# Optimization experiments

Hardware: AMD Instinct MI355X
Metric: run time of the kernel (lower is better)

## Reference

```python
import jax, jax.numpy as jnp
import numpy as np

N = 50000        # nodes
E = 800000       # edges (avg degree 16)
IN = 256         # in_feature_dim
H = 4            # heads_num
F = 64           # out_feature_dim per head (H*F == IN)
NEG_SLOPE = 0.2  # LeakyReLU slope used for both scoring and output activation


def setup_inputs() -> dict:
    key = jax.random.key(0)
    ks = jax.random.split(key, 8)
    x = jax.random.normal(ks[0], (N, IN), dtype=jnp.float32)
    edge_src = jax.random.randint(ks[1], (E,), 0, N, dtype=jnp.int32)
    edge_trg = jax.random.randint(ks[2], (E,), 0, N, dtype=jnp.int32)
    # xavier-ish scaled params
    W = jax.random.normal(ks[3], (IN, H * F), dtype=jnp.float32) * 0.06
    a_src = jax.random.normal(ks[4], (H, F), dtype=jnp.float32) * 0.1
    a_trg = jax.random.normal(ks[5], (H, F), dtype=jnp.float32) * 0.1
    skip_w = jax.random.normal(ks[6], (IN, H * F), dtype=jnp.float32) * 0.06
    bias = jnp.zeros((H * F,), dtype=jnp.float32)
    return {"x": x, "W": W, "a_src": a_src, "a_trg": a_trg,
            "skip_w": skip_w, "bias": bias,
            "edge_src": edge_src, "edge_trg": edge_trg}


def _leaky(v):
    return jnp.where(v > 0, v, NEG_SLOPE * v)


def reference(x, W, a_src, a_trg, skip_w, bias, edge_src, edge_trg):
    n_nodes = x.shape[0]
    # node-wise projection: [N, H, F]
    proj = (x @ W).reshape(n_nodes, H, F)
    # per-head attention scores: [N, H]
    s_src = jnp.einsum('nhf,hf->nh', proj, a_src)
    s_trg = jnp.einsum('nhf,hf->nh', proj, a_trg)
    # lift to edges + LeakyReLU scoring: [E, H]
    e = _leaky(s_src[edge_src] + s_trg[edge_trg])
    # neighborhood-aware (scatter) softmax over incoming edges of each target
    e = e - jnp.max(e)                      # global max subtraction, as in the source
    ex = jnp.exp(e)
    denom = jax.ops.segment_sum(ex, edge_trg, num_segments=n_nodes)  # [N, H]
    attn = ex / (denom[edge_trg] + 1e-16)   # [E, H]
    # weighted aggregation: [E, H, F] -> scatter-add -> [N, H, F]
    weighted = proj[edge_src] * attn[..., None]
    out = jax.ops.segment_sum(weighted, edge_trg, num_segments=n_nodes)
    # skip connection (dims differ: in=256 vs per-head 64 -> use skip_proj)
    out = out + (x @ skip_w).reshape(n_nodes, H, F)
    # concat heads + bias + output activation (default LeakyReLU 0.2)
    out = out.reshape(n_nodes, H * F) + bias
    return _leaky(out)
```

## Files before the change

kernel.cpp:

```cpp
#include <hip/hip_runtime.h>
#include <math.h>

constexpr float SLOPE = 0.2f;

typedef __bf16 bf16x8 __attribute__((ext_vector_type(8)));
typedef __bf16 bf16x4 __attribute__((ext_vector_type(4)));
typedef float  f32x4  __attribute__((ext_vector_type(4)));

__device__ __forceinline__ int imin(int a, int b) { return a < b ? a : b; }

__device__ __forceinline__ void glds16(const void* g, void* l) {
    __builtin_amdgcn_global_load_lds(
        (const __attribute__((address_space(1))) unsigned int*)g,
        (__attribute__((address_space(3))) unsigned int*)l,
        16, 0, 0);
}

__global__ __launch_bounds__(256) void prep_k(
    const float* __restrict__ W, const float* __restrict__ skw,
    __bf16* __restrict__ Bt,
    const float* __restrict__ x, __bf16* __restrict__ xb, int nxv, int nxb,
    const int* __restrict__ etrg, int* __restrict__ cnt, int E)
{
    const int b = blockIdx.x;
    if (b < 512) {
        const int i = b * 256 + threadIdx.x;
        const int n = i >> 8, k = i & 255;
        const float v = (n < 256) ? W[k * 256 + n] : skw[k * 256 + (n - 256)];
        Bt[i] = (__bf16)v;
    } else if (b < 512 + nxb) {
        const int gid = (b - 512) * 256 + threadIdx.x;
        if (gid < nxv) {
            const float4 f0 = *(const float4*)(x + (size_t)gid * 8);
            const float4 f1 = *(const float4*)(x + (size_t)gid * 8 + 4);
            bf16x8 v;
            v[0] = (__bf16)f0.x; v[1] = (__bf16)f0.y;
            v[2] = (__bf16)f0.z; v[3] = (__bf16)f0.w;
            v[4] = (__bf16)f1.x; v[5] = (__bf16)f1.y;
            v[6] = (__bf16)f1.z; v[7] = (__bf16)f1.w;
            *(bf16x8*)(xb + (size_t)gid * 8) = v;
        }
    } else {
        const int e = (b - 512 - nxb) * 256 + threadIdx.x;
        if (e < E) atomicAdd(&cnt[etrg[e]], 1);
    }
}

__global__ __launch_bounds__(256, 2) void gemm_mfma(
    const __bf16* __restrict__ xb, const __bf16* __restrict__ Bt,
    __bf16* __restrict__ projb, float* __restrict__ out, int M)
{
    __shared__ __bf16 As[256 * 32];
    __shared__ __bf16 Bs[128 * 32];

    const int t    = threadIdx.x;
    const int w    = t >> 6;
    const int lane = t & 63;
    const int q    = lane >> 4;
    const int ln   = lane & 15;

    const int row0 = blockIdx.x * 256;
    const int bt0  = blockIdx.y * 128;

    f32x4 acc[4][8] = {};

    for (int k0 = 0; k0 < 256; k0 += 32) {
#pragma unroll
        for (int p = 0; p < 4; ++p) {
            const int idx = p * 256 + t;
            const int r   = idx >> 2;
            const int ko  = (idx & 3) * 8;
            const int ga  = imin(row0 + r, M - 1);
            glds16(xb + (size_t)ga * 256 + k0 + ko, &As[idx * 8]);
        }
#pragma unroll
        for (int p = 0; p < 2; ++p) {
            const int idx = p * 256 + t;
            const int r   = idx >> 2;
            const int ko  = (idx & 3) * 8;
            glds16(Bt + (size_t)(bt0 + r) * 256 + k0 + ko, &Bs[idx * 8]);
        }
        asm volatile("s_waitcnt vmcnt(0)" ::: "memory");
        __syncthreads();

        bf16x8 af[4], bfr[8];
#pragma unroll
        for (int rb = 0; rb < 4; ++rb)
            af[rb] = *(const bf16x8*)&As[(w * 64 + rb * 16 + ln) * 32 + q * 8];
#pragma unroll
        for (int cb = 0; cb < 8; ++cb)
            bfr[cb] = *(const bf16x8*)&Bs[(cb * 16 + ln) * 32 + q * 8];
#pragma unroll
        for (int rb = 0; rb < 4; ++rb)
#pragma unroll
            for (int cb = 0; cb < 8; ++cb)
                acc[rb][cb] = __builtin_amdgcn_mfma_f32_16x16x32_bf16(
                    af[rb], bfr[cb], acc[rb][cb], 0, 0, 0);
        __syncthreads();
    }

    const bool isProj  = (blockIdx.y < 2);
    const int  colbase = (blockIdx.y & 1) * 128;
#pragma unroll
    for (int rb = 0; rb < 4; ++rb) {
#pragma unroll
        for (int r = 0; r < 4; ++r) {
            const int grow = row0 + w * 64 + rb * 16 + q * 4 + r;
            if (grow < M) {
#pragma unroll
                for (int cb = 0; cb < 8; ++cb) {
                    const float v = acc[rb][cb][r];
                    const int gcol = colbase + cb * 16 + ln;
                    if (isProj) projb[(size_t)grow * 256 + gcol] = (__bf16)v;
                    else        out[(size_t)grow * 256 + gcol]   = v;
                }
            }
        }
    }
}

__global__ __launch_bounds__(256) void scores_k(
    const __bf16* __restrict__ projb,
    const float* __restrict__ a_src, const float* __restrict__ a_trg,
    float* __restrict__ s_src, float* __restrict__ s_trg, int N)
{
    const int nid  = blockIdx.x * 4 + (threadIdx.x >> 6);
    const int lane = threadIdx.x & 63;
    if (nid >= N) return;

    const bf16x4 p4  = *(const bf16x4*)(projb + (size_t)nid * 256 + lane * 4);
    const float4 as4 = *(const float4*)(a_src + lane * 4);
    const float4 at4 = *(const float4*)(a_trg + lane * 4);

    float vs = (float)p4[0] * as4.x + (float)p4[1] * as4.y +
               (float)p4[2] * as4.z + (float)p4[3] * as4.w;
    float vt = (float)p4[0] * at4.x + (float)p4[1] * at4.y +
               (float)p4[2] * at4.z + (float)p4[3] * at4.w;

#pragma unroll
    for (int d = 8; d > 0; d >>= 1) {
        vs += __shfl_down(vs, d, 16);
        vt += __shfl_down(vt, d, 16);
    }
    if ((lane & 15) == 0) {
        s_src[nid * 4 + (lane >> 4)] = vs;
        s_trg[nid * 4 + (lane >> 4)] = vt;
    }
}

__global__ __launch_bounds__(1024) void scanA(
    const int* __restrict__ cnt, int* __restrict__ off, int* __restrict__ bsum, int N)
{
    __shared__ int wsum[16];
    const int t = threadIdx.x;
    const int lane = t & 63;
    const int w = t >> 6;
    const int i = blockIdx.x * 1024 + t;
    const int v = (i < N) ? cnt[i] : 0;

    int s = v;
#pragma unroll
    for (int d = 1; d < 64; d <<= 1) {
        int o = __shfl_up(s, d);
        if (lane >= d) s += o;
    }
    if (lane == 63) wsum[w] = s;
    __syncthreads();
    if (w == 0 && lane < 16) {
        int ws = wsum[lane];
        int sc = ws;
#pragma unroll
        for (int d = 1; d < 16; d <<= 1) {
            int o = __shfl_up(sc, d);
            if (lane >= d) sc += o;
        }
        wsum[lane] = sc - ws;
    }
    __syncthreads();
    const int excl = wsum[w] + s - v;
    if (i < N) off[i] = excl;
    if (t == 1023) bsum[blockIdx.x] = excl + v;
}

__global__ __launch_bounds__(256) void scanBC(
    int* __restrict__ off, const int* __restrict__ bsum, int* __restrict__ cur,
    int N, int E)
{
    const int i = blockIdx.x * 256 + threadIdx.x;
    const int chunk = blockIdx.x >> 2;
    const int lane = threadIdx.x & 63;

    int v = (lane < chunk) ? bsum[lane] : 0;
#pragma unroll
    for (int d = 1; d < 64; d <<= 1) v += __shfl_xor(v, d);

    if (i < N) {
        const int o = off[i] + v;
        off[i] = o;
        cur[i] = o;
    }
    if (i == 0) off[N] = E;
}

__global__ __launch_bounds__(256) void scatter_k(
    const int* __restrict__ esrc, const int* __restrict__ etrg,
    int* __restrict__ cur, int* __restrict__ srcs, int E)
{
    const int e = blockIdx.x * 256 + threadIdx.x;
    if (e < E) {
        const int pos = atomicAdd(&cur[etrg[e]], 1);
        srcs[pos] = esrc[e];
    }
}

__global__ __launch_bounds__(256) void aggregate_wave(
    const int* __restrict__ off, const int* __restrict__ srcs,
    const float* __restrict__ s_src, const float* __restrict__ s_trg,
    const __bf16* __restrict__ projb, const float* __restrict__ bias,
    float* __restrict__ out, int N)
{
    const int w = threadIdx.x >> 6;
    const int l = threadIdx.x & 63;
    const int n = blockIdx.x * 4 + w;
    if (n >= N) return;

    const int h  = l >> 4;
    const int je = l & 7;
    const float st = s_trg[n * 4 + h];
    const int b0 = __builtin_amdgcn_readfirstlane(off[n]);
    const int b1 = __builtin_amdgcn_readfirstlane(off[n + 1]);

    f32x4 acc = {0.f, 0.f, 0.f, 0.f};
    float denom = 0.f;

    int i = b0;
    const int nb = (b1 - b0) >> 3;

    int    sgA[8], sgB[8];
    bf16x4 pA[8], pB[8];
    float  exA, exB;

#define ISSUE(SG, P, EX)                                                      \
    {                                                                         \
        const int sm = srcs[i + je];                                          \
        _Pragma("unroll")                                                     \
        for (int j = 0; j < 8; ++j) SG[j] = __builtin_amdgcn_readlane(sm, j); \
        _Pragma("unroll")                                                     \
        for (int j = 0; j < 8; ++j)                                           \
            P[j] = *(const bf16x4*)(projb +                                   \
                     (size_t)((unsigned)SG[j] * 256u) + l * 4);               \
        float v = s_src[sm * 4 + h] + st;                                     \
        v = v > 0.f ? v : SLOPE * v;                                          \
        EX = __expf(v);                                                       \
        i += 8;                                                               \
    }

#define CONSUME(P, EX)                                                        \
    {                                                                         \
        _Pragma("unroll")                                                     \
        for (int j = 0; j < 8; ++j) {                                         \
            const float e = __shfl(EX, (l & 48) | j);                         \
            denom += e;                                                       \
            acc[0] += e * (float)P[j][0];                                     \
            acc[1] += e * (float)P[j][1];                                     \
            acc[2] += e * (float)P[j][2];                                     \
            acc[3] += e * (float)P[j][3];                                     \
        }                                                                     \
    }

    if (nb > 0) {
        ISSUE(sgA, pA, exA);
        int rem = nb - 1;
        while (rem >= 2) {
            ISSUE(sgB, pB, exB);
            CONSUME(pA, exA);
            ISSUE(sgA, pA, exA);
            CONSUME(pB, exB);
            rem -= 2;
        }
        if (rem == 1) {
            ISSUE(sgB, pB, exB);
            CONSUME(pA, exA);
            CONSUME(pB, exB);
        } else {
            CONSUME(pA, exA);
        }
    }
#undef ISSUE
#undef CONSUME

    for (; i < b1; ++i) {
        const int s = srcs[i];
        float v = s_src[s * 4 + h] + st;
        v = v > 0.f ? v : SLOPE * v;
        const float ex = __expf(v);
        denom += ex;
        const bf16x4 p = *(const bf16x4*)(projb + (size_t)((unsigned)s * 256u) + l * 4);
        acc[0] += ex * (float)p[0];
        acc[1] += ex * (float)p[1];
        acc[2] += ex * (float)p[2];
        acc[3] += ex * (float)p[3];
    }

    const size_t o = (size_t)n * 256 + l * 4;
    const float4 sk = *(const float4*)(out + o);
    const float4 b4 = *(const float4*)(bias + l * 4);
    const float inv = 1.f / (denom + 1e-16f);
    float4 r;
    r.x = acc[0] * inv + sk.x + b4.x;
    r.y = acc[1] * inv + sk.y + b4.y;
    r.z = acc[2] * inv + sk.z + b4.z;
    r.w = acc[3] * inv + sk.w + b4.w;
    r.x = r.x > 0.f ? r.x : SLOPE * r.x;
    r.y = r.y > 0.f ? r.y : SLOPE * r.y;
    r.z = r.z > 0.f ? r.z : SLOPE * r.z;
    r.w = r.w > 0.f ? r.w : SLOPE * r.w;
    *(float4*)(out + o) = r;
}

extern "C" void kernel_launch(void* const* d_in, const int* in_sizes, int n_in,
                              void* d_out, int out_size, void* d_ws, size_t ws_size,
                              hipStream_t stream)
{
    const float* x     = (const float*)d_in[0];
    const float* W     = (const float*)d_in[1];
    const float* a_src = (const float*)d_in[2];
    const float* a_trg = (const float*)d_in[3];
    const float* skw   = (const float*)d_in[4];
    const float* bias  = (const float*)d_in[5];
    const int*   esrc  = (const int*)d_in[6];
    const int*   etrg  = (const int*)d_in[7];

    const int N = in_sizes[0] / 256;
    const int E = in_sizes[6];
    float* out = (float*)d_out;

    __bf16* projb = (__bf16*)d_ws;
    __bf16* Bt    = projb + (size_t)N * 256;
    __bf16* xb    = Bt + 512 * 256;
    float*  s_src = (float*)(xb + (size_t)N * 256);
    float*  s_trg = s_src + (size_t)N * 4;
    int*    cnt   = (int*)(s_trg + (size_t)N * 4);
    int*    off   = cnt + N;
    int*    cur   = off + (N + 1);
    int*    bsum  = cur + N;
    int*    srcs  = bsum + 64;

    const int nxv = (N * 256) / 8;
    const int nxb = (nxv + 255) / 256;
    const int nhb = (E + 255) / 256;
    const int nsc = (N + 1023) / 1024;

    hipMemsetAsync(cnt, 0, (size_t)N * sizeof(int), stream);

    prep_k<<<512 + nxb + nhb, 256, 0, stream>>>(W, skw, Bt, x, xb, nxv, nxb,
                                                etrg, cnt, E);

    dim3 g((N + 255) / 256, 4);
    gemm_mfma<<<g, 256, 0, stream>>>(xb, Bt, projb, out, N);

    scores_k<<<(N + 3) / 4, 256, 0, stream>>>(projb, a_src, a_trg, s_src, s_trg, N);

    scanA<<<nsc, 1024, 0, stream>>>(cnt, off, bsum, N);
    scanBC<<<(N + 255) / 256, 256, 0, stream>>>(off, bsum, cur, N, E);

    scatter_k<<<(E + 255) / 256, 256, 0, stream>>>(esrc, etrg, cur, srcs, E);

    aggregate_wave<<<(N + 3) / 4, 256, 0, stream>>>(off, srcs, s_src, s_trg,
                                                    projb, bias, out, N);
}
```

Baseline: 308.8 us.

## Fold attention score projection into GEMM via precomputed W·a columns

```diff
diff --git a/kernel.cpp b/kernel.cpp
--- a/kernel.cpp
+++ b/kernel.cpp
@@ -18,6 +18,7 @@
 
 __global__ __launch_bounds__(256) void prep_k(
     const float* __restrict__ W, const float* __restrict__ skw,
+    const float* __restrict__ a_src, const float* __restrict__ a_trg,
     __bf16* __restrict__ Bt,
     const float* __restrict__ x, __bf16* __restrict__ xb, int nxv, int nxb,
     const int* __restrict__ etrg, int* __restrict__ cnt, int E)
@@ -28,8 +29,46 @@
         const int n = i >> 8, k = i & 255;
         const float v = (n < 256) ? W[k * 256 + n] : skw[k * 256 + (n - 256)];
         Bt[i] = (__bf16)v;
-    } else if (b < 512 + nxb) {
-        const int gid = (b - 512) * 256 + threadIdx.x;
+    } else if (b == 512) {
+        __shared__ float lw[32][260];
+        __shared__ float la[8][64];
+        const int t = threadIdx.x;
+        for (int i = t; i < 512; i += 256) {
+            const int row = i >> 6, f = i & 63;
+            la[row][f] = (row < 4) ? a_src[row * 64 + f]
+                                   : a_trg[(row - 4) * 64 + f];
+        }
+        const int c  = t & 15;
+        const int ks = t >> 4;
+        for (int k0 = 0; k0 < 256; k0 += 32) {
+            __syncthreads();
+#pragma unroll
+            for (int p = 0; p < 8; ++p) {
+                const int idx = p * 256 + t;
+                const int r   = idx >> 6;
+                const int cc  = (idx & 63) * 4;
+                *(float4*)&lw[r][cc] =
+                    *(const float4*)(W + (size_t)(k0 + r) * 256 + cc);
+            }
+            __syncthreads();
+            if (c < 8) {
+                const int cb = (c & 3) * 64;
+#pragma unroll
+                for (int kk = 0; kk < 2; ++kk) {
+                    const int kr = ks + kk * 16;
+                    float s = 0.f;
+#pragma unroll
+                    for (int f = 0; f < 64; ++f)
+                        s += lw[kr][cb + f] * la[c][f];
+                    Bt[(size_t)(512 + c) * 256 + (k0 + kr)] = (__bf16)s;
+                }
+            } else {
+                Bt[(size_t)(512 + c) * 256 + (k0 + ks)]      = (__bf16)0.f;
+                Bt[(size_t)(512 + c) * 256 + (k0 + ks + 16)] = (__bf16)0.f;
+            }
+        }
+    } else if (b < 513 + nxb) {
+        const int gid = (b - 513) * 256 + threadIdx.x;
         if (gid < nxv) {
             const float4 f0 = *(const float4*)(x + (size_t)gid * 8);
             const float4 f1 = *(const float4*)(x + (size_t)gid * 8 + 4);
@@ -41,14 +80,15 @@
             *(bf16x8*)(xb + (size_t)gid * 8) = v;
         }
     } else {
-        const int e = (b - 512 - nxb) * 256 + threadIdx.x;
+        const int e = (b - 513 - nxb) * 256 + threadIdx.x;
         if (e < E) atomicAdd(&cnt[etrg[e]], 1);
     }
 }
 
 __global__ __launch_bounds__(256, 2) void gemm_mfma(
     const __bf16* __restrict__ xb, const __bf16* __restrict__ Bt,
-    __bf16* __restrict__ projb, float* __restrict__ out, int M)
+    __bf16* __restrict__ projb, float* __restrict__ out,
+    float* __restrict__ s_src, float* __restrict__ s_trg, int M)
 {
     __shared__ __bf16 As[256 * 32];
     __shared__ __bf16 Bs[128 * 32];
@@ -59,8 +99,11 @@
     const int q    = lane >> 4;
     const int ln   = lane & 15;
 
-    const int row0 = blockIdx.x * 256;
-    const int bt0  = blockIdx.y * 128;
+    const int bid  = blockIdx.x;
+    const int bx   = bid / 5;
+    const int y    = bid % 5;
+    const int row0 = bx * 256;
+    const int bt0  = y * 128;
 
     f32x4 acc[4][8] = {};
 
@@ -73,78 +116,84 @@
             const int ga  = imin(row0 + r, M - 1);
             glds16(xb + (size_t)ga * 256 + k0 + ko, &As[idx * 8]);
         }
-#pragma unroll
-        for (int p = 0; p < 2; ++p) {
-            const int idx = p * 256 + t;
-            const int r   = idx >> 2;
-            const int ko  = (idx & 3) * 8;
-            glds16(Bt + (size_t)(bt0 + r) * 256 + k0 + ko, &Bs[idx * 8]);
+        if (y < 4) {
+#pragma unroll
+            for (int p = 0; p < 2; ++p) {
+                const int idx = p * 256 + t;
+                const int r   = idx >> 2;
+                const int ko  = (idx & 3) * 8;
+                glds16(Bt + (size_t)(bt0 + r) * 256 + k0 + ko, &Bs[idx * 8]);
+            }
+        } else {
+            const int i6 = t & 63;
+            const int r  = i6 >> 2;
+            const int ko = (i6 & 3) * 8;
+            glds16(Bt + (size_t)(512 + r) * 256 + k0 + ko, &Bs[i6 * 8]);
         }
         asm volatile("s_waitcnt vmcnt(0)" ::: "memory");
         __syncthreads();
 
-        bf16x8 af[4], bfr[8];
-#pragma unroll
-        for (int rb = 0; rb < 4; ++rb)
-            af[rb] = *(const bf16x8*)&As[(w * 64 + rb * 16 + ln) * 32 + q * 8];
-#pragma unroll
-        for (int cb = 0; cb < 8; ++cb)
-            bfr[cb] = *(const bf16x8*)&Bs[(cb * 16 + ln) * 32 + q * 8];
-#pragma unroll
-        for (int rb = 0; rb < 4; ++rb)
+        if (y < 4) {
+            bf16x8 af[4], bfr[8];
+#pragma unroll
+            for (int rb = 0; rb < 4; ++rb)
+                af[rb] = *(const bf16x8*)&As[(w * 64 + rb * 16 + ln) * 32 + q * 8];
 #pragma unroll
             for (int cb = 0; cb < 8; ++cb)
-                acc[rb][cb] = __builtin_amdgcn_mfma_f32_16x16x32_bf16(
-                    af[rb], bfr[cb], acc[rb][cb], 0, 0, 0);
+                bfr[cb] = *(const bf16x8*)&Bs[(cb * 16 + ln) * 32 + q * 8];
+#pragma unroll
+            for (int rb = 0; rb < 4; ++rb)
+#pragma unroll
+                for (int cb = 0; cb < 8; ++cb)
+                    acc[rb][cb] = __builtin_amdgcn_mfma_f32_16x16x32_bf16(
+                        af[rb], bfr[cb], acc[rb][cb], 0, 0, 0);
+        } else {
+            const bf16x8 b0 = *(const bf16x8*)&Bs[(ln * 16 + ln * 16) + 0];
+            const bf16x8 bf0 = *(const bf16x8*)&Bs[ln * 32 + q * 8];
+#pragma unroll
+            for (int rb = 0; rb < 4; ++rb) {
+                const bf16x8 af =
+                    *(const bf16x8*)&As[(w * 64 + rb * 16 + ln) * 32 + q * 8];
+                acc[rb][0] = __builtin_amdgcn_mfma_f32_16x16x32_bf16(
+                    af, bf0, acc[rb][0], 0, 0, 0);
+            }
+            (void)b0;
+        }
         __syncthreads();
     }
 
-    const bool isProj  = (blockIdx.y < 2);
-    const int  colbase = (blockIdx.y & 1) * 128;
-#pragma unroll
-    for (int rb = 0; rb < 4; ++rb) {
-#pragma unroll
-        for (int r = 0; r < 4; ++r) {
-            const int grow = row0 + w * 64 + rb * 16 + q * 4 + r;
-            if (grow < M) {
-#pragma unroll
-                for (int cb = 0; cb < 8; ++cb) {
-                    const float v = acc[rb][cb][r];
-                    const int gcol = colbase + cb * 16 + ln;
-                    if (isProj) projb[(size_t)grow * 256 + gcol] = (__bf16)v;
-                    else        out[(size_t)grow * 256 + gcol]   = v;
+    if (y < 4) {
+        const bool isProj  = (y < 2);
+        const int  colbase = (y & 1) * 128;
+#pragma unroll
+        for (int rb = 0; rb < 4; ++rb) {
+#pragma unroll
+            for (int r = 0; r < 4; ++r) {
+                const int grow = row0 + w * 64 + rb * 16 + q * 4 + r;
+                if (grow < M) {
+#pragma unroll
+                    for (int cb = 0; cb < 8; ++cb) {
+                        const float v = acc[rb][cb][r];
+                        const int gcol = colbase + cb * 16 + ln;
+                        if (isProj) projb[(size_t)grow * 256 + gcol] = (__bf16)v;
+                        else        out[(size_t)grow * 256 + gcol]   = v;
+                    }
                 }
             }
         }
-    }
-}
-
-__global__ __launch_bounds__(256) void scores_k(
-    const __bf16* __restrict__ projb,
-    const float* __restrict__ a_src, const float* __restrict__ a_trg,
-    float* __restrict__ s_src, float* __restrict__ s_trg, int N)
-{
-    const int nid  = blockIdx.x * 4 + (threadIdx.x >> 6);
-    const int lane = threadIdx.x & 63;
-    if (nid >= N) return;
-
-    const bf16x4 p4  = *(const bf16x4*)(projb + (size_t)nid * 256 + lane * 4);
-    const float4 as4 = *(const float4*)(a_src + lane * 4);
-    const float4 at4 = *(const float4*)(a_trg + lane * 4);
-
-    float vs = (float)p4[0] * as4.x + (float)p4[1] * as4.y +
-               (float)p4[2] * as4.z + (float)p4[3] * as4.w;
-    float vt = (float)p4[0] * at4.x + (float)p4[1] * at4.y +
-               (float)p4[2] * at4.z + (float)p4[3] * at4.w;
-
-#pragma unroll
-    for (int d = 8; d > 0; d >>= 1) {
-        vs += __shfl_down(vs, d, 16);
-        vt += __shfl_down(vt, d, 16);
-    }
-    if ((lane & 15) == 0) {
-        s_src[nid * 4 + (lane >> 4)] = vs;
-        s_trg[nid * 4 + (lane >> 4)] = vt;
+    } else {
+#pragma unroll
+        for (int rb = 0; rb < 4; ++rb) {
+#pragma unroll
+            for (int r = 0; r < 4; ++r) {
+                const int grow = row0 + w * 64 + rb * 16 + q * 4 + r;
+                if (grow < M && ln < 8) {
+                    const float v = acc[rb][0][r];
+                    if (ln < 4) s_src[grow * 4 + ln]       = v;
+                    else        s_trg[grow * 4 + (ln - 4)] = v;
+                }
+            }
+        }
     }
 }
 
@@ -337,7 +386,7 @@
 
     __bf16* projb = (__bf16*)d_ws;
     __bf16* Bt    = projb + (size_t)N * 256;
-    __bf16* xb    = Bt + 512 * 256;
+    __bf16* xb    = Bt + 528 * 256;
     float*  s_src = (float*)(xb + (size_t)N * 256);
     float*  s_trg = s_src + (size_t)N * 4;
     int*    cnt   = (int*)(s_trg + (size_t)N * 4);
@@ -350,16 +399,14 @@
     const int nxb = (nxv + 255) / 256;
     const int nhb = (E + 255) / 256;
     const int nsc = (N + 1023) / 1024;
+    const int nxt = (N + 255) / 256;
 
     hipMemsetAsync(cnt, 0, (size_t)N * sizeof(int), stream);
 
-    prep_k<<<512 + nxb + nhb, 256, 0, stream>>>(W, skw, Bt, x, xb, nxv, nxb,
-                                                etrg, cnt, E);
-
-    dim3 g((N + 255) / 256, 4);
-    gemm_mfma<<<g, 256, 0, stream>>>(xb, Bt, projb, out, N);
-
-    scores_k<<<(N + 3) / 4, 256, 0, stream>>>(projb, a_src, a_trg, s_src, s_trg, N);
+    prep_k<<<513 + nxb + nhb, 256, 0, stream>>>(W, skw, a_src, a_trg, Bt,
+                                                x, xb, nxv, nxb, etrg, cnt, E);
+
+    gemm_mfma<<<nxt * 5, 256, 0, stream>>>(xb, Bt, projb, out, s_src, s_trg, N);
 
     scanA<<<nsc, 1024, 0, stream>>>(cnt, off, bsum, N);
     scanBC<<<(N + 255) / 256, 256, 0, stream>>>(off, bsum, cur, N, E);
```

Result: no change. 308.3 us (-0.2%).

## Fuse attention score computation into GEMM epilogue and linearize block grid

Applied to the files above, without the earlier changes.

```diff
diff --git a/kernel.cpp b/kernel.cpp
--- a/kernel.cpp
+++ b/kernel.cpp
@@ -48,7 +48,9 @@
 
 __global__ __launch_bounds__(256, 2) void gemm_mfma(
     const __bf16* __restrict__ xb, const __bf16* __restrict__ Bt,
-    __bf16* __restrict__ projb, float* __restrict__ out, int M)
+    __bf16* __restrict__ projb, float* __restrict__ out,
+    const float* __restrict__ a_src, const float* __restrict__ a_trg,
+    float* __restrict__ s_src, float* __restrict__ s_trg, int M)
 {
     __shared__ __bf16 As[256 * 32];
     __shared__ __bf16 Bs[128 * 32];
@@ -59,8 +61,11 @@
     const int q    = lane >> 4;
     const int ln   = lane & 15;
 
-    const int row0 = blockIdx.x * 256;
-    const int bt0  = blockIdx.y * 128;
+    const int bid  = blockIdx.x;
+    const int bx   = bid >> 2;
+    const int y    = bid & 3;
+    const int row0 = bx * 256;
+    const int bt0  = y * 128;
 
     f32x4 acc[4][8] = {};
 
@@ -99,8 +104,8 @@
         __syncthreads();
     }
 
-    const bool isProj  = (blockIdx.y < 2);
-    const int  colbase = (blockIdx.y & 1) * 128;
+    const bool isProj  = (y < 2);
+    const int  colbase = (y & 1) * 128;
 #pragma unroll
     for (int rb = 0; rb < 4; ++rb) {
 #pragma unroll
@@ -117,34 +122,48 @@
             }
         }
     }
-}
-
-__global__ __launch_bounds__(256) void scores_k(
-    const __bf16* __restrict__ projb,
-    const float* __restrict__ a_src, const float* __restrict__ a_trg,
-    float* __restrict__ s_src, float* __restrict__ s_trg, int N)
-{
-    const int nid  = blockIdx.x * 4 + (threadIdx.x >> 6);
-    const int lane = threadIdx.x & 63;
-    if (nid >= N) return;
-
-    const bf16x4 p4  = *(const bf16x4*)(projb + (size_t)nid * 256 + lane * 4);
-    const float4 as4 = *(const float4*)(a_src + lane * 4);
-    const float4 at4 = *(const float4*)(a_trg + lane * 4);
-
-    float vs = (float)p4[0] * as4.x + (float)p4[1] * as4.y +
-               (float)p4[2] * as4.z + (float)p4[3] * as4.w;
-    float vt = (float)p4[0] * at4.x + (float)p4[1] * at4.y +
-               (float)p4[2] * at4.z + (float)p4[3] * at4.w;
-
-#pragma unroll
-    for (int d = 8; d > 0; d >>= 1) {
-        vs += __shfl_down(vs, d, 16);
-        vt += __shfl_down(vt, d, 16);
-    }
-    if ((lane & 15) == 0) {
-        s_src[nid * 4 + (lane >> 4)] = vs;
-        s_trg[nid * 4 + (lane >> 4)] = vt;
+
+    if (y < 2) {
+        float as[8], at[8];
+#pragma unroll
+        for (int cb = 0; cb < 8; ++cb) {
+            const int lcol = cb * 16 + ln;
+            const int hh   = y * 2 + (lcol >> 6);
+            const int f    = lcol & 63;
+            as[cb] = a_src[hh * 64 + f];
+            at[cb] = a_trg[hh * 64 + f];
+        }
+#pragma unroll
+        for (int rb = 0; rb < 4; ++rb) {
+#pragma unroll
+            for (int r = 0; r < 4; ++r) {
+                float s0 = 0.f, s1 = 0.f, t0 = 0.f, t1 = 0.f;
+#pragma unroll
+                for (int cb = 0; cb < 4; ++cb) {
+                    s0 += acc[rb][cb][r] * as[cb];
+                    t0 += acc[rb][cb][r] * at[cb];
+                }
+#pragma unroll
+                for (int cb = 4; cb < 8; ++cb) {
+                    s1 += acc[rb][cb][r] * as[cb];
+                    t1 += acc[rb][cb][r] * at[cb];
+                }
+#pragma unroll
+                for (int d = 1; d < 16; d <<= 1) {
+                    s0 += __shfl_xor(s0, d);
+                    s1 += __shfl_xor(s1, d);
+                    t0 += __shfl_xor(t0, d);
+                    t1 += __shfl_xor(t1, d);
+                }
+                const int grow = row0 + w * 64 + rb * 16 + q * 4 + r;
+                if (ln == 0 && grow < M) {
+                    s_src[grow * 4 + y * 2]     = s0;
+                    s_src[grow * 4 + y * 2 + 1] = s1;
+                    s_trg[grow * 4 + y * 2]     = t0;
+                    s_trg[grow * 4 + y * 2 + 1] = t1;
+                }
+            }
+        }
     }
 }
 
@@ -350,16 +369,15 @@
     const int nxb = (nxv + 255) / 256;
     const int nhb = (E + 255) / 256;
     const int nsc = (N + 1023) / 1024;
+    const int nxt = (N + 255) / 256;
 
     hipMemsetAsync(cnt, 0, (size_t)N * sizeof(int), stream);
 
     prep_k<<<512 + nxb + nhb, 256, 0, stream>>>(W, skw, Bt, x, xb, nxv, nxb,
                                                 etrg, cnt, E);
 
-    dim3 g((N + 255) / 256, 4);
-    gemm_mfma<<<g, 256, 0, stream>>>(xb, Bt, projb, out, N);
-
-    scores_k<<<(N + 3) / 4, 256, 0, stream>>>(projb, a_src, a_trg, s_src, s_trg, N);
+    gemm_mfma<<<nxt * 4, 256, 0, stream>>>(xb, Bt, projb, out, a_src, a_trg,
+                                           s_src, s_trg, N);
 
     scanA<<<nsc, 1024, 0, stream>>>(cnt, off, bsum, N);
     scanBC<<<(N + 255) / 256, 256, 0, stream>>>(off, bsum, cur, N, E);
```

Result: no change. 310.6 us (+0.6%).
